# Kernel tuning notes

Hardware: AMD Instinct MI355X
Metric: run time of the kernel (lower is better)

## Reference

```python
import jax, jax.numpy as jnp
import numpy as np

EPS = 1e-5
BLOCKS = 8

def _bn(x, g, b, m, v):
    # eval-mode BatchNorm1d over channel dim of [B, C, T]
    return g[:, None] * (x - m[:, None]) * jax.lax.rsqrt(v[:, None] + EPS) + b[:, None]

def _conv1x1(x, w):
    # x: [B, Cin, T], w: [Cout, Cin] -> [B, Cout, T]
    return jnp.einsum('bct,oc->bot', x, w)

def _dwconv(x, w, dil):
    # x: [B, C, T], w: [C, K] depthwise dilated conv, 'same' padding
    C, K = w.shape
    pad = dil * (K - 1) // 2
    return jax.lax.conv_general_dilated(
        x, w[:, None, :], window_strides=(1,), padding=[(pad, pad)],
        rhs_dilation=(dil,), dimension_numbers=('NCH', 'OIH', 'NCH'),
        feature_group_count=C)

def setup_inputs() -> dict:
    key = jax.random.key(0)
    ks = jax.random.split(key, 16)
    B, Cb, H, T, K = 16, 256, 512, 4096, 3
    d = {}
    d['x'] = jax.random.normal(ks[0], (B, Cb, T), jnp.float32)
    d['bn1_gamma'] = jax.random.uniform(ks[1], (BLOCKS, Cb), jnp.float32)
    d['bn1_beta'] = jax.random.normal(ks[2], (BLOCKS, Cb), jnp.float32)
    d['bn1_mean'] = jax.random.normal(ks[3], (BLOCKS, Cb), jnp.float32)
    d['bn1_var'] = jax.random.uniform(ks[4], (BLOCKS, Cb), jnp.float32)
    d['w1'] = jax.random.normal(ks[5], (BLOCKS, H, Cb), jnp.float32)
    d['bn2_gamma'] = jax.random.uniform(ks[6], (BLOCKS, H), jnp.float32)
    d['bn2_beta'] = jax.random.normal(ks[7], (BLOCKS, H), jnp.float32)
    d['bn2_mean'] = jax.random.normal(ks[8], (BLOCKS, H), jnp.float32)
    d['bn2_var'] = jax.random.uniform(ks[9], (BLOCKS, H), jnp.float32)
    d['dw_w'] = jax.random.normal(ks[10], (BLOCKS, H, K), jnp.float32)
    d['bn3_gamma'] = jax.random.uniform(ks[11], (BLOCKS, H), jnp.float32)
    d['bn3_beta'] = jax.random.normal(ks[12], (BLOCKS, H), jnp.float32)
    d['bn3_mean'] = jax.random.normal(ks[13], (BLOCKS, H), jnp.float32)
    d['bn3_var'] = jax.random.uniform(ks[14], (BLOCKS, H), jnp.float32)
    d['w2'] = jax.random.normal(ks[15], (BLOCKS, Cb, H), jnp.float32)
    return d

def reference(x, bn1_gamma, bn1_beta, bn1_mean, bn1_var, w1,
              bn2_gamma, bn2_beta, bn2_mean, bn2_var, dw_w,
              bn3_gamma, bn3_beta, bn3_mean, bn3_var, w2):
    sign = jnp.sign  # binary activation on inputs and weights
    resid = x
    for i in range(BLOCKS):
        dil = 2 ** i
        h = _bn(resid, bn1_gamma[i], bn1_beta[i], bn1_mean[i], bn1_var[i])
        h = _conv1x1(sign(h), sign(w1[i]))                 # 1x1, Cb -> H
        h = _bn(h, bn2_gamma[i], bn2_beta[i], bn2_mean[i], bn2_var[i])
        h = _dwconv(sign(h), sign(dw_w[i]), dil)           # depthwise dilated
        h = _bn(h, bn3_gamma[i], bn3_beta[i], bn3_mean[i], bn3_var[i])
        h = _conv1x1(sign(h), sign(w2[i]))                 # 1x1, H -> Cb
        resid = resid + h
    return resid
```

## Files before the change

kernel.cpp:

```cpp
#include <hip/hip_runtime.h>
#include <stdint.h>

namespace {
constexpr int Bn  = 16;
constexpr int Cc  = 256;
constexpr int Hn  = 512;
constexpr int Tn  = 4096;
constexpr int CWn = Cc / 32;
constexpr int HWn = Hn / 32;
constexpr int TWn = Tn / 32;
constexpr int TC  = 64;
constexpr float EPSf = 1e-5f;
}

typedef __attribute__((ext_vector_type(4)))  int i32x4;
typedef __attribute__((ext_vector_type(16))) int i32x16;

__global__ __launch_bounds__(256) void setup_kernel(
    const float* __restrict__ bn1g, const float* __restrict__ bn1b,
    const float* __restrict__ bn1m, const float* __restrict__ bn1v,
    const float* __restrict__ w1,
    const float* __restrict__ bn2g, const float* __restrict__ bn2b,
    const float* __restrict__ bn2m, const float* __restrict__ bn2v,
    const float* __restrict__ dww,
    const float* __restrict__ bn3g, const float* __restrict__ bn3b,
    const float* __restrict__ bn3m, const float* __restrict__ bn3v,
    const float* __restrict__ w2,
    float* __restrict__ thr1, float* __restrict__ thr2, float* __restrict__ thr3,
    uint32_t* __restrict__ dws, uint32_t* __restrict__ W1p, uint32_t* __restrict__ W2p,
    uint8_t* __restrict__ W1u, int* __restrict__ Sw1, int* __restrict__ T2i)
{
  const int idx = blockIdx.x * 256 + threadIdx.x;
  if (idx < 8 * Hn * CWn) {
    const int w = idx & (CWn - 1);
    const int h = idx >> 3;
    const float* src = w1 + (size_t)h * Cc + w * 32;
    uint32_t word = 0;
#pragma unroll
    for (int j = 0; j < 32; ++j) word |= (uint32_t)(src[j] > 0.f) << j;
    W1p[h * CWn + w] = word;
    atomicAdd(&Sw1[h], (int)__popc(word));
    uint32_t* dst = (uint32_t*)(W1u + (size_t)h * 256);
#pragma unroll
    for (int q = 0; q < 8; ++q) {
      const uint32_t dw = (((word >> (4 * q)) & 0xFu) * 0x00204081u) & 0x01010101u;
      const int off = (w * 32 + q * 4) ^ ((h & 15) << 4);
      dst[off >> 2] = dw;
    }
  } else {
    const int k = idx - 8 * Hn * CWn;
    const int w = k & (HWn - 1);
    const int c = k >> 4;
    const float* src = w2 + (size_t)c * Hn + w * 32;
    uint32_t word = 0;
#pragma unroll
    for (int j = 0; j < 32; ++j) word |= (uint32_t)(src[j] > 0.f) << j;
    W2p[c * HWn + w] = word;
  }
  if (idx < 8 * Cc)
    thr1[idx] = bn1m[idx] - bn1b[idx] * sqrtf(bn1v[idx] + EPSf) / bn1g[idx];
  if (idx < 8 * Hn) {
    const float th2 = bn2m[idx] - bn2b[idx] * sqrtf(bn2v[idx] + EPSf) / bn2g[idx];
    thr2[idx] = th2;
    int T;
    if (th2 >= 8.0e6f)       T =  (1 << 24);
    else if (th2 <= -8.0e6f) T = -(1 << 24);
    else if (th2 == th2)     T = (int)floorf(th2) + 1;
    else                     T =  (1 << 24);
    T2i[idx] = T;
    thr3[idx] = bn3m[idx] - bn3b[idx] * sqrtf(bn3v[idx] + EPSf) / bn3g[idx];
    uint32_t dw = 0;
    for (int k2 = 0; k2 < 3; ++k2) dw |= (uint32_t)(dww[(size_t)idx * 3 + k2] > 0.f) << k2;
    dws[idx] = dw;
  }
}

__global__ __launch_bounds__(256) void k1_pack(
    const float* __restrict__ resid, const float* __restrict__ thr1,
    uint32_t* __restrict__ Xp)
{
  const int idx = blockIdx.x * 256 + threadIdx.x;
  const int t  = idx & (Tn - 1);
  const int cw = (idx >> 12) & (CWn - 1);
  const int b  = idx >> 15;
  const float* r = resid + ((size_t)(b * Cc + cw * 32)) * Tn + t;
  uint32_t word = 0;
#pragma unroll
  for (int j = 0; j < 32; ++j)
    word |= (uint32_t)(r[(size_t)j * Tn] > thr1[cw * 32 + j]) << j;
  Xp[((size_t)b * CWn + cw) * Tn + t] = word;
}

__global__ __launch_bounds__(256) void k2_gemm1(
    const uint32_t* __restrict__ Xp, const uint32_t* __restrict__ W1p,
    const float* __restrict__ thr2, uint32_t* __restrict__ Y)
{
  const int bid  = blockIdx.x;
  const int tblk = bid & 15;
  const int og   = (bid >> 4) & 63;
  const int b    = bid >> 10;
  const int t    = tblk * 256 + threadIdx.x;
  const int o    = og * 8;

  const uint32_t* xrow = Xp + (size_t)b * CWn * Tn + t;
  const uint32_t* wrow = W1p + o * CWn;
  int acc[8] = {0, 0, 0, 0, 0, 0, 0, 0};
#pragma unroll
  for (int w = 0; w < CWn; ++w) {
    const uint32_t xw = xrow[(size_t)w * Tn];
#pragma unroll
    for (int r = 0; r < 8; ++r)
      acc[r] += __popc(xw ^ wrow[r * CWn + w]);
  }
  const int lane = threadIdx.x & 63;
#pragma unroll
  for (int r = 0; r < 8; ++r) {
    const float v = (float)(Cc - 2 * acc[r]);
    const uint64_t m = __ballot(v > thr2[o + r]);
    if ((lane & 31) == 0)
      Y[((size_t)b * TWn + (t >> 5)) * Hn + o + r] = (uint32_t)(m >> lane);
  }
}

__global__ __launch_bounds__(512) void k_iter(
    const uint32_t* __restrict__ Yin, const uint32_t* __restrict__ dws,
    const float* __restrict__ thr3, const uint32_t* __restrict__ W2p,
    const float* __restrict__ rin, float* __restrict__ rout,
    const float* __restrict__ thr1n,
    const uint8_t* __restrict__ W1u_n, const int* __restrict__ Sw1_n,
    const int* __restrict__ T2i_n, uint32_t* __restrict__ Yout,
    int dil, int do_next)
{
  __shared__ uint32_t Zlds[HWn * TC];
  __shared__ __align__(16) uint8_t Xi8[TC * 256];
  __shared__ __align__(16) uint8_t Wbuf[128 * 256];
  __shared__ int Sx[TC];
  __shared__ int Tc[Hn];

  const int chunk = blockIdx.x & (Tn / TC - 1);
  const int b     = blockIdx.x >> 6;
  const int tid   = threadIdx.x;
  const int lane  = tid & 63;
  const int wid   = __builtin_amdgcn_readfirstlane(tid >> 6);
  const int lh    = lane & 31;
  const int twL   = lane >> 5;
  const int tw0   = chunk * 2;

  if (tid < TC) Sx[tid] = 0;

#pragma unroll
  for (int task = 0; task < 2; ++task) {
    const int hw = wid * 2 + task;
    const int tw = tw0 + twL;
    const int ch = hw * 32 + lh;

    const uint32_t* yb = Yin + (size_t)b * TWn * Hn + ch;
    const uint32_t ycur = yb[(size_t)tw * Hn];
    uint32_t yl, yr, Vl, Vr;
    if (dil >= 32) {
      const int dw = dil >> 5;
      const bool lok = tw >= dw, rok = tw + dw < TWn;
      yl = lok ? yb[(size_t)(tw - dw) * Hn] : 0u;
      yr = rok ? yb[(size_t)(tw + dw) * Hn] : 0u;
      Vl = lok ? ~0u : 0u;
      Vr = rok ? ~0u : 0u;
    } else {
      const uint32_t yp = (tw > 0) ? yb[(size_t)(tw - 1) * Hn] : 0u;
      const uint32_t yn = (tw < TWn - 1) ? yb[(size_t)(tw + 1) * Hn] : 0u;
      yl = (ycur << dil) | ((tw > 0) ? (yp >> (32 - dil)) : 0u);
      yr = (ycur >> dil) | ((tw < TWn - 1) ? (yn << (32 - dil)) : 0u);
      Vl = (tw == 0) ? (~0u << dil) : ~0u;
      Vr = (tw == TWn - 1) ? (~0u >> dil) : ~0u;
    }
    const uint32_t d = dws[ch];
    const uint32_t a  = ((d & 1u) ? yl : ~yl) & Vl;
    const uint32_t bb = (d & 2u) ? ycur : ~ycur;
    const uint32_t c  = ((d & 4u) ? yr : ~yr) & Vr;

    const float thr = thr3[ch];
    const float v3 = (thr + 3.f) * 0.5f;
    const float v2 = (thr + 2.f) * 0.5f;
    const int K3 = (int)(v3 >= 0.f) + (int)(v3 >= 1.f) + (int)(v3 >= 2.f) + (int)(v3 >= 3.f);
    const int K2 = (int)(v2 >= 0.f) + (int)(v2 >= 1.f) + (int)(v2 >= 2.f);

    const uint32_t g1 = a | bb | c;
    const uint32_t g2 = (a & bb) | (c & (a | bb));
    const uint32_t g3 = a & bb & c;
    const uint32_t full = (K3 == 0) ? ~0u : (K3 == 1) ? g1 : (K3 == 2) ? g2
                        : (K3 == 3) ? g3 : 0u;
    const uint32_t lm = (K2 == 0) ? ~0u : (K2 == 1) ? (bb | c) : (K2 == 2) ? (bb & c) : 0u;
    const uint32_t rm = (K2 == 0) ? ~0u : (K2 == 1) ? (a | bb) : (K2 == 2) ? (a & bb) : 0u;

    uint32_t w = (Vl & Vr & full) | (~Vl & lm) | (~Vr & rm);

#pragma unroll
    for (int s = 16; s; s >>= 1) {
      const uint32_t m = 0xFFFFFFFFu / ((1u << s) + 1u);
      const uint32_t o = __shfl_xor(w, s, 64);
      w = ((lane & s) == 0) ? ((w & m) | ((o & m) << s))
                            : ((w & ~m) | ((o & ~m) >> s));
    }
    Zlds[hw * TC + twL * 32 + lh] = w;
  }
  __syncthreads();

  {
    const int cw = wid;
    const int tl = lane;
    const int tg = chunk * TC + tl;

    uint32_t z[HWn];
#pragma unroll
    for (int w = 0; w < HWn; ++w) z[w] = Zlds[w * TC + tl];

    const uint32_t* wrow = W2p + (cw * 32) * HWn;
    const size_t base = ((size_t)(b * Cc + cw * 32)) * Tn + tg;
    const float* rp = rin + base;
    float* op = rout + base;
    const int swz = (tl & 15) << 4;
    uint32_t word = 0;
#pragma unroll 1
    for (int jo = 0; jo < 32; jo += 8) {
      float rv[8];
#pragma unroll
      for (int jj = 0; jj < 8; ++jj)
        rv[jj] = rp[(size_t)(jo + jj) * Tn];
      uint32_t blo = 0, bhi = 0;
#pragma unroll
      for (int jj = 0; jj < 8; ++jj) {
        const int j = jo + jj;
        int acc = 0;
#pragma unroll
        for (int w = 0; w < HWn; ++w) acc += __popc(z[w] ^ wrow[j * HWn + w]);
        const float ro = rv[jj] + (float)(Hn - 2 * acc);
        op[(size_t)j * Tn] = ro;
        const uint32_t bit = (uint32_t)(ro > thr1n[cw * 32 + j]);
        word |= bit << j;
        if (jj < 4) blo |= bit << (jj * 8);
        else        bhi |= bit << ((jj - 4) * 8);
      }
      const int c0 = cw * 32 + jo;
      *(uint32_t*)&Xi8[tl * 256 + (c0 ^ swz)]     = blo;
      *(uint32_t*)&Xi8[tl * 256 + (c0 ^ swz) + 4] = bhi;
    }
    atomicAdd(&Sx[tl], (int)__popc(word));
  }
  __syncthreads();

  if (do_next) {
    Tc[tid] = T2i_n[tid] + 2 * Sw1_n[tid] - 256;

    const int ntile = wid & 1;
    const int mloc  = wid >> 1;
    const int tloc  = ntile * 32 + (lane & 31);
    const int half  = lane >> 5;

    i32x4 bf[8];
#pragma unroll
    for (int ks = 0; ks < 8; ++ks) {
      const int koff = (ks * 32 + half * 16) ^ ((tloc & 15) << 4);
      bf[ks] = *(const i32x4*)&Xi8[tloc * 256 + koff];
    }
    const int Sxv2 = 2 * Sx[tloc];
    uint32_t* yo = Yout + ((size_t)b * TWn + (chunk * 2 + ntile)) * Hn;

#pragma unroll 1
    for (int msup = 0; msup < 4; ++msup) {
      const uint32_t* gsrc = (const uint32_t*)(W1u_n + msup * 32768);
      uint32_t* ldst = (uint32_t*)Wbuf;
      i32x4 stg[4];
#pragma unroll
      for (int s = 0; s < 4; ++s)
        stg[s] = *(const i32x4*)&gsrc[(s * 512 + tid) * 4];
#pragma unroll
      for (int s = 0; s < 4; ++s)
        *(i32x4*)&ldst[(s * 512 + tid) * 4] = stg[s];
      __syncthreads();

      const int lrow = mloc * 32 + (lane & 31);
      i32x16 acc = {0,0,0,0, 0,0,0,0, 0,0,0,0, 0,0,0,0};
#pragma unroll
      for (int ks = 0; ks < 8; ++ks) {
        const int aoff = (ks * 32 + half * 16) ^ ((lrow & 15) << 4);
        const i32x4 af = *(const i32x4*)&Wbuf[lrow * 256 + aoff];
        acc = __builtin_amdgcn_mfma_i32_32x32x32_i8(af, bf[ks], acc, 0, 0, 0);
      }

      const int obase = msup * 128 + mloc * 32;
#pragma unroll
      for (int r = 0; r < 16; ++r) {
        const int row = (r & 3) + 8 * (r >> 2) + 4 * half;
        const int o = obase + row;
        const uint64_t m = __ballot((acc[r] << 2) >= Tc[o] + Sxv2);
        if ((lane & 31) == 0) yo[o] = (uint32_t)(m >> lane);
      }
      __syncthreads();
    }
  }
}

extern "C" void kernel_launch(void* const* d_in, const int* in_sizes, int n_in,
                              void* d_out, int out_size, void* d_ws, size_t ws_size,
                              hipStream_t stream)
{
  const float* x     = (const float*)d_in[0];
  const float* bn1g  = (const float*)d_in[1];
  const float* bn1b  = (const float*)d_in[2];
  const float* bn1m  = (const float*)d_in[3];
  const float* bn1v  = (const float*)d_in[4];
  const float* w1    = (const float*)d_in[5];
  const float* bn2g  = (const float*)d_in[6];
  const float* bn2b  = (const float*)d_in[7];
  const float* bn2m  = (const float*)d_in[8];
  const float* bn2v  = (const float*)d_in[9];
  const float* dww   = (const float*)d_in[10];
  const float* bn3g  = (const float*)d_in[11];
  const float* bn3b  = (const float*)d_in[12];
  const float* bn3m  = (const float*)d_in[13];
  const float* bn3v  = (const float*)d_in[14];
  const float* w2    = (const float*)d_in[15];
  float* out = (float*)d_out;

  char* ws = (char*)d_ws;
  uint32_t* Xp  = (uint32_t*)(ws);
  uint32_t* Ya  = (uint32_t*)(ws + (2u  << 20));
  uint32_t* Yb  = (uint32_t*)(ws + (6u  << 20));
  uint32_t* W1p = (uint32_t*)(ws + (10u << 20));
  uint32_t* W2p = (uint32_t*)(ws + (10u << 20) + (128u << 10));
  float*    thr1 = (float*)(ws + (10u << 20) + (256u << 10));
  float*    thr2 = thr1 + 8 * Cc;
  float*    thr3 = thr2 + 8 * Hn;
  uint32_t* dws  = (uint32_t*)(thr3 + 8 * Hn);
  uint8_t*  W1u  = (uint8_t*)(ws + (11u << 20));
  int*      Sw1  = (int*)(ws + (12u << 20));
  int*      T2i  = (int*)(ws + (12u << 20) + (16u << 10));

  hipMemsetAsync(Sw1, 0, 8 * Hn * sizeof(int), stream);

  setup_kernel<<<256, 256, 0, stream>>>(bn1g, bn1b, bn1m, bn1v, w1,
                                        bn2g, bn2b, bn2m, bn2v, dww,
                                        bn3g, bn3b, bn3m, bn3v, w2,
                                        thr1, thr2, thr3, dws, W1p, W2p,
                                        W1u, Sw1, T2i);

  k1_pack <<<2048,  256, 0, stream>>>(x, thr1, Xp);
  k2_gemm1<<<16384, 256, 0, stream>>>(Xp, W1p, thr2, Ya);

  for (int i = 0; i < 8; ++i) {
    const float* rin = (i == 0) ? x : out;
    const int inext = (i < 7) ? i + 1 : 7;
    const uint32_t* Yin  = (i & 1) ? Yb : Ya;
    uint32_t*       Yout = (i & 1) ? Ya : Yb;
    k_iter<<<1024, 512, 0, stream>>>(Yin, dws + i * Hn, thr3 + i * Hn,
                                     W2p + i * Cc * HWn, rin, out,
                                     thr1 + inext * Cc,
                                     W1u + (size_t)inext * Hn * 256,
                                     Sw1 + inext * Hn, T2i + inext * Hn,
                                     Yout, 1 << i, (i < 7) ? 1 : 0);
  }
}
```

Before: 382.2 us.

## Compute second binary 1x1 conv with int8 MFMA instead of XOR-popcount

The H->Cb binary conv in k_iter now unpacks the sign bits of the depthwise output into 0/1 int8 bytes in LDS and multiplies them against a pre-unpacked 0/1 int8 copy of w2 using 32x32x32 i8 MFMA. The XNOR count is recovered algebraically from the dot product plus popcounts of the activations and weights. This replaces the scalar popcount loop with matrix-core work. It adds a larger LDS buffer, reused for the next-block W1 staging, more setup packing, and per-row Sz atomics.

```diff
diff --git a/kernel.cpp b/kernel.cpp
--- a/kernel.cpp
+++ b/kernel.cpp
@@ -27,8 +27,9 @@
     const float* __restrict__ bn3m, const float* __restrict__ bn3v,
     const float* __restrict__ w2,
     float* __restrict__ thr1, float* __restrict__ thr2, float* __restrict__ thr3,
-    uint32_t* __restrict__ dws, uint32_t* __restrict__ W1p, uint32_t* __restrict__ W2p,
-    uint8_t* __restrict__ W1u, int* __restrict__ Sw1, int* __restrict__ T2i)
+    uint32_t* __restrict__ dws, uint32_t* __restrict__ W1p,
+    uint8_t* __restrict__ W1u, int* __restrict__ Sw1, int* __restrict__ T2i,
+    uint8_t* __restrict__ W2uf, int* __restrict__ Sw2)
 {
   const int idx = blockIdx.x * 256 + threadIdx.x;
   if (idx < 8 * Hn * CWn) {
@@ -55,7 +56,14 @@
     uint32_t word = 0;
 #pragma unroll
     for (int j = 0; j < 32; ++j) word |= (uint32_t)(src[j] > 0.f) << j;
-    W2p[c * HWn + w] = word;
+    atomicAdd(&Sw2[c], (int)__popc(word));
+    const int blk = c >> 8, cl = c & 255;
+    uint32_t* dst = (uint32_t*)(W2uf + (size_t)blk * 131072);
+#pragma unroll
+    for (int q = 0; q < 8; ++q) {
+      const uint32_t dw = (((word >> (4 * q)) & 0xFu) * 0x00204081u) & 0x01010101u;
+      dst[((w * 2 + (q >> 2)) * 256 + cl) * 4 + (q & 3)] = dw;
+    }
   }
   if (idx < 8 * Cc)
     thr1[idx] = bn1m[idx] - bn1b[idx] * sqrtf(bn1v[idx] + EPSf) / bn1g[idx];
@@ -124,18 +132,20 @@
 
 __global__ __launch_bounds__(512) void k_iter(
     const uint32_t* __restrict__ Yin, const uint32_t* __restrict__ dws,
-    const float* __restrict__ thr3, const uint32_t* __restrict__ W2p,
+    const float* __restrict__ thr3,
+    const uint8_t* __restrict__ W2uf, const int* __restrict__ Sw2_i,
     const float* __restrict__ rin, float* __restrict__ rout,
     const float* __restrict__ thr1n,
     const uint8_t* __restrict__ W1u_n, const int* __restrict__ Sw1_n,
     const int* __restrict__ T2i_n, uint32_t* __restrict__ Yout,
     int dil, int do_next)
 {
-  __shared__ uint32_t Zlds[HWn * TC];
+  __shared__ __align__(16) uint8_t ZW[TC * 512];
   __shared__ __align__(16) uint8_t Xi8[TC * 256];
-  __shared__ __align__(16) uint8_t Wbuf[128 * 256];
-  __shared__ int Sx[TC];
-  __shared__ int Tc[Hn];
+  __shared__ int   Tc[Hn];
+  __shared__ float thr1L[Cc];
+  __shared__ int   Sw2x2L[Cc];
+  __shared__ int   Sx[TC], Sz[TC];
 
   const int chunk = blockIdx.x & (Tn / TC - 1);
   const int b     = blockIdx.x >> 6;
@@ -146,7 +156,9 @@
   const int twL   = lane >> 5;
   const int tw0   = chunk * 2;
 
-  if (tid < TC) Sx[tid] = 0;
+  if (tid < TC) { Sx[tid] = 0; Sz[tid] = 0; }
+  if (tid < Cc) { thr1L[tid] = thr1n[tid]; Sw2x2L[tid] = 2 * Sw2_i[tid]; }
+  __syncthreads();
 
 #pragma unroll
   for (int task = 0; task < 2; ++task) {
@@ -200,50 +212,72 @@
       w = ((lane & s) == 0) ? ((w & m) | ((o & m) << s))
                             : ((w & ~m) | ((o & ~m) >> s));
     }
-    Zlds[hw * TC + twL * 32 + lh] = w;
+    const int swzA = (lane & 15) << 4;
+    uint32_t e[8];
+#pragma unroll
+    for (int q = 0; q < 8; ++q)
+      e[q] = (((w >> (4 * q)) & 0xFu) * 0x00204081u) & 0x01010101u;
+    i32x4 v0; v0[0] = e[0]; v0[1] = e[1]; v0[2] = e[2]; v0[3] = e[3];
+    i32x4 v1; v1[0] = e[4]; v1[1] = e[5]; v1[2] = e[6]; v1[3] = e[7];
+    *(i32x4*)&ZW[lane * 512 + ((hw * 32)      ^ swzA)] = v0;
+    *(i32x4*)&ZW[lane * 512 + ((hw * 32 + 16) ^ swzA)] = v1;
+    atomicAdd(&Sz[lane], (int)__popc(w));
   }
   __syncthreads();
 
   {
-    const int cw = wid;
-    const int tl = lane;
-    const int tg = chunk * TC + tl;
-
-    uint32_t z[HWn];
-#pragma unroll
-    for (int w = 0; w < HWn; ++w) z[w] = Zlds[w * TC + tl];
-
-    const uint32_t* wrow = W2p + (cw * 32) * HWn;
-    const size_t base = ((size_t)(b * Cc + cw * 32)) * Tn + tg;
-    const float* rp = rin + base;
-    float* op = rout + base;
-    const int swz = (tl & 15) << 4;
-    uint32_t word = 0;
-#pragma unroll 1
-    for (int jo = 0; jo < 32; jo += 8) {
-      float rv[8];
-#pragma unroll
-      for (int jj = 0; jj < 8; ++jj)
-        rv[jj] = rp[(size_t)(jo + jj) * Tn];
-      uint32_t blo = 0, bhi = 0;
-#pragma unroll
-      for (int jj = 0; jj < 8; ++jj) {
-        const int j = jo + jj;
-        int acc = 0;
-#pragma unroll
-        for (int w = 0; w < HWn; ++w) acc += __popc(z[w] ^ wrow[j * HWn + w]);
-        const float ro = rv[jj] + (float)(Hn - 2 * acc);
-        op[(size_t)j * Tn] = ro;
-        const uint32_t bit = (uint32_t)(ro > thr1n[cw * 32 + j]);
-        word |= bit << j;
-        if (jj < 4) blo |= bit << (jj * 8);
-        else        bhi |= bit << ((jj - 4) * 8);
-      }
-      const int c0 = cw * 32 + jo;
-      *(uint32_t*)&Xi8[tl * 256 + (c0 ^ swz)]     = blo;
-      *(uint32_t*)&Xi8[tl * 256 + (c0 ^ swz) + 4] = bhi;
-    }
-    atomicAdd(&Sx[tl], (int)__popc(word));
+    const int mc   = wid;
+    const int half = lane >> 5;
+    const int lrow = mc * 32 + lh;
+    const int t0   = chunk * TC;
+
+    float rv0[16], rv1[16];
+#pragma unroll
+    for (int r = 0; r < 16; ++r) {
+      const int cr = mc * 32 + (r & 3) + 8 * (r >> 2) + 4 * half;
+      const float* rowp = rin + ((size_t)(b * Cc + cr)) * Tn + t0;
+      rv0[r] = rowp[lh];
+      rv1[r] = rowp[32 + lh];
+    }
+
+    const int swz0 = (lh & 15) << 4;
+    i32x16 acc0 = {0,0,0,0, 0,0,0,0, 0,0,0,0, 0,0,0,0};
+    i32x16 acc1 = {0,0,0,0, 0,0,0,0, 0,0,0,0, 0,0,0,0};
+#pragma unroll
+    for (int ks = 0; ks < 16; ++ks) {
+      const int k0 = ks * 32 + half * 16;
+      const i32x4 af  = *(const i32x4*)(W2uf + (((size_t)(ks * 2 + half) * 256 + lrow) * 16));
+      const i32x4 bf0 = *(const i32x4*)&ZW[lh * 512 + (k0 ^ swz0)];
+      const i32x4 bf1 = *(const i32x4*)&ZW[(32 + lh) * 512 + (k0 ^ swz0)];
+      acc0 = __builtin_amdgcn_mfma_i32_32x32x32_i8(af, bf0, acc0, 0, 0, 0);
+      acc1 = __builtin_amdgcn_mfma_i32_32x32x32_i8(af, bf1, acc1, 0, 0, 0);
+    }
+
+    const int Sz0 = 2 * Sz[lh], Sz1 = 2 * Sz[32 + lh];
+    uint32_t dw0[4] = {0,0,0,0}, dw1[4] = {0,0,0,0};
+#pragma unroll
+    for (int r = 0; r < 16; ++r) {
+      const int cr = mc * 32 + (r & 3) + 8 * (r >> 2) + 4 * half;
+      const int sw2 = Sw2x2L[cr];
+      const float th = thr1L[cr];
+      float* orow = rout + ((size_t)(b * Cc + cr)) * Tn + t0;
+      const float ro0 = rv0[r] + (float)((acc0[r] << 2) - Sz0 - sw2 + 512);
+      const float ro1 = rv1[r] + (float)((acc1[r] << 2) - Sz1 - sw2 + 512);
+      orow[lh]      = ro0;
+      orow[32 + lh] = ro1;
+      dw0[r >> 2] |= (uint32_t)(ro0 > th) << ((r & 3) * 8);
+      dw1[r >> 2] |= (uint32_t)(ro1 > th) << ((r & 3) * 8);
+    }
+    int cnt0 = 0, cnt1 = 0;
+#pragma unroll
+    for (int g = 0; g < 4; ++g) {
+      const int cb = mc * 32 + g * 8 + half * 4;
+      *(uint32_t*)&Xi8[lh * 256 + (cb ^ swz0)]        = dw0[g];
+      *(uint32_t*)&Xi8[(32 + lh) * 256 + (cb ^ swz0)] = dw1[g];
+      cnt0 += __popc(dw0[g]); cnt1 += __popc(dw1[g]);
+    }
+    atomicAdd(&Sx[lh], cnt0);
+    atomicAdd(&Sx[32 + lh], cnt1);
   }
   __syncthreads();
 
@@ -267,7 +301,7 @@
 #pragma unroll 1
     for (int msup = 0; msup < 4; ++msup) {
       const uint32_t* gsrc = (const uint32_t*)(W1u_n + msup * 32768);
-      uint32_t* ldst = (uint32_t*)Wbuf;
+      uint32_t* ldst = (uint32_t*)ZW;
       i32x4 stg[4];
 #pragma unroll
       for (int s = 0; s < 4; ++s)
@@ -282,7 +316,7 @@
 #pragma unroll
       for (int ks = 0; ks < 8; ++ks) {
         const int aoff = (ks * 32 + half * 16) ^ ((lrow & 15) << 4);
-        const i32x4 af = *(const i32x4*)&Wbuf[lrow * 256 + aoff];
+        const i32x4 af = *(const i32x4*)&ZW[lrow * 256 + aoff];
         acc = __builtin_amdgcn_mfma_i32_32x32x32_i8(af, bf[ks], acc, 0, 0, 0);
       }
 
@@ -326,22 +360,23 @@
   uint32_t* Ya  = (uint32_t*)(ws + (2u  << 20));
   uint32_t* Yb  = (uint32_t*)(ws + (6u  << 20));
   uint32_t* W1p = (uint32_t*)(ws + (10u << 20));
-  uint32_t* W2p = (uint32_t*)(ws + (10u << 20) + (128u << 10));
   float*    thr1 = (float*)(ws + (10u << 20) + (256u << 10));
   float*    thr2 = thr1 + 8 * Cc;
   float*    thr3 = thr2 + 8 * Hn;
   uint32_t* dws  = (uint32_t*)(thr3 + 8 * Hn);
   uint8_t*  W1u  = (uint8_t*)(ws + (11u << 20));
   int*      Sw1  = (int*)(ws + (12u << 20));
-  int*      T2i  = (int*)(ws + (12u << 20) + (16u << 10));
-
-  hipMemsetAsync(Sw1, 0, 8 * Hn * sizeof(int), stream);
+  int*      Sw2  = (int*)(ws + (12u << 20) + (16u << 10));
+  int*      T2i  = (int*)(ws + (12u << 20) + (24u << 10));
+  uint8_t*  W2uf = (uint8_t*)(ws + (13u << 20));
+
+  hipMemsetAsync(Sw1, 0, (24u << 10), stream);
 
   setup_kernel<<<256, 256, 0, stream>>>(bn1g, bn1b, bn1m, bn1v, w1,
                                         bn2g, bn2b, bn2m, bn2v, dww,
                                         bn3g, bn3b, bn3m, bn3v, w2,
-                                        thr1, thr2, thr3, dws, W1p, W2p,
-                                        W1u, Sw1, T2i);
+                                        thr1, thr2, thr3, dws, W1p,
+                                        W1u, Sw1, T2i, W2uf, Sw2);
 
   k1_pack <<<2048,  256, 0, stream>>>(x, thr1, Xp);
   k2_gemm1<<<16384, 256, 0, stream>>>(Xp, W1p, thr2, Ya);
@@ -352,7 +387,8 @@
     const uint32_t* Yin  = (i & 1) ? Yb : Ya;
     uint32_t*       Yout = (i & 1) ? Ya : Yb;
     k_iter<<<1024, 512, 0, stream>>>(Yin, dws + i * Hn, thr3 + i * Hn,
-                                     W2p + i * Cc * HWn, rin, out,
+                                     W2uf + (size_t)i * 131072, Sw2 + i * Cc,
+                                     rin, out,
                                      thr1 + inext * Cc,
                                      W1u + (size_t)inext * Hn * 256,
                                      Sw1 + inext * Hn, T2i + inext * Hn,
```

Measured after the change: 376.8 us. Within noise of the previous version (-1.4%).
